# Kernel tuning notes

Hardware: AMD Instinct MI355X
Metric: run time of the kernel (lower is better)

## Reference

```python
import jax, jax.numpy as jnp
import numpy as np

VOCAB = 100000
EMBED = 300
HIDDEN = 300
BATCH = 32768
K_NEG = 10
N_CLASSES = 2
EPS = 1e-5
DENO_W = 1.0
CONO_W = 1.0


def setup_inputs() -> dict:
    key = jax.random.key(0)
    ks = jax.random.split(key, 12)
    init_range = 1.0 / EMBED
    return {
        "center_word_ids": jax.random.randint(ks[0], (BATCH,), 0, VOCAB),
        "context_word_ids": jax.random.randint(ks[1], (BATCH,), 0, VOCAB),
        "neg_context_ids": jax.random.randint(ks[2], (BATCH, K_NEG), 0, VOCAB),
        "party_label": jax.random.randint(ks[3], (BATCH,), 0, N_CLASSES),
        "center_emb": jax.random.uniform(ks[4], (VOCAB, EMBED), jnp.float32, -init_range, init_range),
        "context_emb": jax.random.normal(ks[5], (VOCAB, EMBED), jnp.float32) * 0.02,
        "W_enc": jax.random.normal(ks[6], (HIDDEN, EMBED), jnp.float32) * (1.0 / np.sqrt(EMBED)),
        "b_enc": jnp.zeros((HIDDEN,), jnp.float32),
        "W_dec": jax.random.normal(ks[7], (EMBED, HIDDEN), jnp.float32) * (1.0 / np.sqrt(HIDDEN)),
        "b_dec": jnp.zeros((EMBED,), jnp.float32),
        "W_cls": jax.random.normal(ks[8], (N_CLASSES, HIDDEN), jnp.float32) * (1.0 / np.sqrt(HIDDEN)),
        "b_cls": jnp.zeros((N_CLASSES,), jnp.float32),
    }


def reference(center_word_ids, context_word_ids, neg_context_ids, party_label,
              center_emb, context_emb, W_enc, b_enc, W_dec, b_dec, W_cls, b_cls):
    # encoder_forward (dropout p=0 -> identity)
    emb = center_emb[center_word_ids]                      # [B, E]
    enc = emb @ W_enc.T + b_enc                            # [B, H]
    # deno_forward: skip-gram negative sampling
    center_v = enc @ W_dec.T + b_dec                       # [B, E]
    ctx_v = context_emb[context_word_ids]                  # [B, E]
    pos_score = jnp.clip(jnp.sum(center_v * ctx_v, axis=1), -10.0, 10.0)
    pos = -jax.nn.log_sigmoid(pos_score)                   # [B]
    neg_v = context_emb[neg_context_ids]                   # [B, K, E]
    neg_score = jnp.clip(jnp.einsum('bke,be->bk', neg_v, center_v), -10.0, 10.0)
    neg = -jnp.sum(jax.nn.log_sigmoid(-neg_score), axis=1)  # [B]
    deno_loss = jnp.clip(jnp.mean(pos + neg), EPS, 10.0)
    # cono_forward + cross entropy
    logits = enc @ W_cls.T + b_cls                         # [B, C]
    logp = jax.nn.log_softmax(logits, axis=-1)
    nll = -jnp.take_along_axis(logp, party_label[:, None], axis=1)[:, 0]
    cono_loss = jnp.clip(jnp.mean(nll), EPS, 10.0)
    encoder_loss = jnp.clip(DENO_W * deno_loss + CONO_W * cono_loss, EPS, None)
    return jnp.stack([encoder_loss, deno_loss, cono_loss])
```

## Files before the change

### kernel.cpp

```cpp
#include <hip/hip_runtime.h>
#include <math.h>

#define VOCAB   100000
#define EMBED   300
#define HIDDEN  300
#define BATCH   32768
#define K_NEG   10
#define EPSV    1e-5f

#define KPAD      320
#define NPAD      384
#define CV_STRIDE 304
#define CTX8_STRIDE 304
#define WC2_STRIDE 304
#define FP8_SCALE 64.0f
#define FP8_DESCALE 0.015625f
#define NBUCKET 512

typedef __attribute__((ext_vector_type(8))) short  short8;
typedef __attribute__((ext_vector_type(4))) float  f32x4;
typedef __attribute__((ext_vector_type(2))) float  floatx2;

#if defined(__has_builtin)
#if __has_builtin(__builtin_amdgcn_cvt_pk_f32_fp8) && __has_builtin(__builtin_amdgcn_cvt_pk_fp8_f32)
#define HAVE_CVT_FP8 1
#endif
#endif

__device__ inline float b2f(unsigned short u) {
    union { unsigned int i; float f; } v; v.i = ((unsigned int)u) << 16; return v.f;
}
__device__ inline unsigned short f2b(float f) {
    union { float f; unsigned int i; } v; v.f = f;
    unsigned int r = v.i + 0x7FFFu + ((v.i >> 16) & 1u);
    return (unsigned short)(r >> 16);
}
__device__ inline void up2(unsigned int u, float& lo, float& hi) {
    union { unsigned int i; float f; } a, b;
    a.i = u << 16; b.i = u & 0xFFFF0000u;
    lo = a.f; hi = b.f;
}
__device__ inline float softplus_fast(float x) {
    const float t = __builtin_amdgcn_exp2f(fabsf(x) * -1.44269504f);
    const float l = __builtin_amdgcn_logf(1.f + t) * 0.69314718f;
    return fmaxf(x, 0.f) + l;
}

__device__ inline float fp8_to_f(unsigned int u8) {
    const unsigned s = (u8 >> 7) & 1, e = (u8 >> 3) & 15, m = u8 & 7;
    float v;
    if (e) { union { unsigned i; float f; } b; b.i = ((e + 120u) << 23) | (m << 20); v = b.f; }
    else v = (float)m * 0.001953125f;
    return s ? -v : v;
}
__device__ inline unsigned char f_to_fp8(float x) {
    union { float f; unsigned i; } b; b.f = x;
    const unsigned s = (b.i >> 31) << 7;
    const float a = fabsf(x);
    if (a >= 440.f) return (unsigned char)(s | 0x7E);
    if (a < 0.015625f) {
        int m = (int)rintf(a * 512.f);
        return (unsigned char)(m >= 8 ? (s | 0x08) : (s | (unsigned)m));
    }
    unsigned r = (b.i & 0x7FFFFFFFu) + 0x7FFFFu + ((b.i >> 20) & 1u);
    unsigned e8 = (r >> 23) - 120u;
    unsigned m8 = (r >> 20) & 7u;
    if (e8 > 15u) return (unsigned char)(s | 0x7E);
    return (unsigned char)(s | (e8 << 3) | m8);
}
__device__ inline unsigned enc4fp8(float a, float b, float c, float d) {
#ifdef HAVE_CVT_FP8
    int v = 0;
    v = __builtin_amdgcn_cvt_pk_fp8_f32(a, b, v, false);
    v = __builtin_amdgcn_cvt_pk_fp8_f32(c, d, v, true);
    return (unsigned)v;
#else
    return (unsigned)f_to_fp8(a) | ((unsigned)f_to_fp8(b) << 8) |
           ((unsigned)f_to_fp8(c) << 16) | ((unsigned)f_to_fp8(d) << 24);
#endif
}
__device__ inline void dec4fp8(unsigned u, float* f) {
#ifdef HAVE_CVT_FP8
    floatx2 lo = __builtin_amdgcn_cvt_pk_f32_fp8((int)u, false);
    floatx2 hi = __builtin_amdgcn_cvt_pk_f32_fp8((int)u, true);
    f[0] = lo[0]; f[1] = lo[1]; f[2] = hi[0]; f[3] = hi[1];
#else
    f[0] = fp8_to_f(u); f[1] = fp8_to_f(u >> 8);
    f[2] = fp8_to_f(u >> 16); f[3] = fp8_to_f(u >> 24);
#endif
}

__device__ inline void load_lds16(const void* g, void* l) {
    __builtin_amdgcn_global_load_lds(
        (const __attribute__((address_space(1))) unsigned int*)g,
        (__attribute__((address_space(3))) unsigned int*)l, 16, 0, 0);
}

__device__ inline float red64(float v) {
    #pragma unroll
    for (int m = 32; m; m >>= 1) v += __shfl_xor(v, m);
    return v;
}

#define CH1 (BATCH * 75)
#define CH2 (VOCAB * 75)
#define CHTOT (CH1 + CH2)
#define PREP_BLOCKS 2048

__global__ __launch_bounds__(256)
void prep_kernel(const float* __restrict__ cemb, const int* __restrict__ cids,
                 const float* __restrict__ xemb,
                 unsigned short* __restrict__ emb_b, unsigned char* __restrict__ ctx8)
{
    const unsigned GT = PREP_BLOCKS * 256;
    for (unsigned base = blockIdx.x * 256 + threadIdx.x; base < CHTOT; base += GT * 4) {
        float4 v[4];
        unsigned c[4];
        bool ok[4];
        #pragma unroll
        for (int u = 0; u < 4; ++u) {
            c[u] = base + u * GT;
            ok[u] = (c[u] < CHTOT);
            if (ok[u]) {
                unsigned cc = c[u];
                if (cc < CH1) {
                    const unsigned row = cc / 75, e = cc - row * 75;
                    v[u] = *(const float4*)(cemb + (size_t)cids[row] * 300 + e * 4);
                } else {
                    cc -= CH1;
                    const unsigned row = cc / 75, e = cc - row * 75;
                    v[u] = *(const float4*)(xemb + (size_t)row * 300 + e * 4);
                }
            }
        }
        #pragma unroll
        for (int u = 0; u < 4; ++u) {
            if (!ok[u]) continue;
            unsigned cc = c[u];
            if (cc < CH1) {
                const unsigned row = cc / 75, e = cc - row * 75;
                uint2 d;
                d.x = (unsigned)f2b(v[u].x) | ((unsigned)f2b(v[u].y) << 16);
                d.y = (unsigned)f2b(v[u].z) | ((unsigned)f2b(v[u].w) << 16);
                char* dst = (char*)emb_b + (size_t)row * (KPAD * 2) + e * 8;
                if (e < 74) {
                    *(uint2*)dst = d;
                } else {
                    *(uint4*)dst = make_uint4(d.x, d.y, 0u, 0u);
                    char* rb = (char*)emb_b + (size_t)row * (KPAD * 2);
                    *(uint4*)(rb + 608) = make_uint4(0u, 0u, 0u, 0u);
                    *(uint4*)(rb + 624) = make_uint4(0u, 0u, 0u, 0u);
                }
            } else {
                cc -= CH1;
                const unsigned row = cc / 75, e = cc - row * 75;
                const unsigned enc = enc4fp8(v[u].x * FP8_SCALE, v[u].y * FP8_SCALE,
                                             v[u].z * FP8_SCALE, v[u].w * FP8_SCALE);
                char* dst = (char*)ctx8 + (size_t)row * CTX8_STRIDE + e * 4;
                if (e < 74) {
                    *(unsigned*)dst = enc;
                } else {
                    *(uint2*)dst = make_uint2(enc, 0u);
                }
            }
        }
    }
}

__global__ __launch_bounds__(256)
void w2_kernel(const float* __restrict__ Wd, const float* __restrict__ We,
               unsigned short* __restrict__ w2p)
{
    __shared__ float ds[16][33];
    __shared__ float es[32][17];
    const int tid = threadIdx.x;
    const int tn = tid >> 4, tk = tid & 15;
    const int n = blockIdx.y * 16 + tn;
    const int k = blockIdx.x * 16 + tk;

    float acc = 0.f;
    for (int h0 = 0; h0 < 300; h0 += 32) {
        {
            const int i = tid * 2;
            const int a = i >> 5, h = i & 31;
            const int rr = blockIdx.y * 16 + a;
            #pragma unroll
            for (int j = 0; j < 2; ++j) {
                const int hh = h + j;
                ds[a][hh] = (rr < 300 && h0 + hh < 300) ? Wd[rr * 300 + h0 + hh] : 0.f;
            }
        }
        {
            const int i = tid * 2;
            const int h = i >> 4, c = i & 15;
            const int cc = blockIdx.x * 16 + c;
            #pragma unroll
            for (int j = 0; j < 2; ++j)
                es[h][c + j] = (h0 + h < 300 && cc + j < 300) ? We[(h0 + h) * 300 + cc + j] : 0.f;
        }
        __syncthreads();
        #pragma unroll
        for (int h = 0; h < 32; ++h)
            acc = fmaf(ds[tn][h], es[h][tk], acc);
        __syncthreads();
    }
    if (n < NPAD && k < KPAD)
        w2p[n * KPAD + k] = (n < 300 && k < 300) ? f2b(acc) : (unsigned short)0;
}

__global__ __launch_bounds__(256)
void wb_kernel(const float* __restrict__ Wd, const float* __restrict__ We,
               const float* __restrict__ Wc, const float* __restrict__ b_enc,
               const float* __restrict__ b_dec, const float* __restrict__ b_cls,
               float* __restrict__ wc2, float* __restrict__ bias2, float* __restrict__ bc2)
{
    const int unit = blockIdx.x * 4 + (threadIdx.x >> 6);
    const int lane = threadIdx.x & 63;
    if (unit >= 914) return;
    float s = 0.f;
    if (unit < 304) {
        const int c = unit;
        if (c < 300)
            for (int k = lane; k < 300; k += 64) s = fmaf(Wd[c * 300 + k], b_enc[k], s);
        s = red64(s);
        if (lane == 0) bias2[c] = (c < 300) ? s + b_dec[c] : 0.f;
    } else if (unit < 912) {
        const int u2 = unit - 304;
        const int j = u2 >= 304 ? 1 : 0;
        const int c = u2 - j * 304;
        if (c < 300)
            for (int h = lane; h < 300; h += 64) s = fmaf(Wc[j * 300 + h], We[h * 300 + c], s);
        s = red64(s);
        if (lane == 0) wc2[j * WC2_STRIDE + c] = s;
    } else {
        const int j = unit - 912;
        for (int h = lane; h < 300; h += 64) s = fmaf(Wc[j * 300 + h], b_enc[h], s);
        s = red64(s);
        if (lane == 0) bc2[j] = s + b_cls[j];
    }
}

__global__ __launch_bounds__(256)
void gemm_cv_kernel(const unsigned short* __restrict__ A,
                    const unsigned short* __restrict__ B,
                    const float* __restrict__ bias,
                    unsigned short* __restrict__ C)
{
    __shared__ unsigned short As[2][128 * 32];
    __shared__ unsigned short Bs[2][128 * 32];

    const int tid  = threadIdx.x;
    const int wave = tid >> 6;
    const int lane = tid & 63;
    const int m0 = blockIdx.y * 128;
    const int n0 = blockIdx.x * 128;

    const int wr = (wave & 1) * 64;
    const int wc = (wave >> 1) * 64;
    const int fr = lane & 15;
    const int fq = lane >> 4;

    const unsigned short* gA[2];
    const unsigned short* gB[2];
    int ldsOff[2];
    #pragma unroll
    for (int inst = 0; inst < 2; ++inst) {
        const int t = wave * 2 + inst;
        const int r = (t << 4) + (lane >> 2);
        const int c = ((lane & 3) - r - (r >> 2)) & 3;
        gA[inst] = A + (size_t)(m0 + r) * KPAD + c * 8;
        gB[inst] = B + (size_t)(n0 + r) * KPAD + c * 8;
        ldsOff[inst] = t << 9;
    }

    int aoff[4], boff[4];
    #pragma unroll
    for (int i = 0; i < 4; ++i) {
        const int ra = wr + i * 16 + fr;
        aoff[i] = (ra << 5) + (((fq + ra + (ra >> 2)) & 3) << 3);
        const int rb = wc + i * 16 + fr;
        boff[i] = (rb << 5) + (((fq + rb + (rb >> 2)) & 3) << 3);
    }

    f32x4 acc[4][4] = {};

    #pragma unroll
    for (int inst = 0; inst < 2; ++inst) {
        load_lds16(gA[inst], &As[0][ldsOff[inst]]);
        load_lds16(gB[inst], &Bs[0][ldsOff[inst]]);
    }

    int cur = 0;
    for (int ki = 0; ki < KPAD / 32; ++ki) {
        __syncthreads();
        if (ki + 1 < KPAD / 32) {
            const int k0 = (ki + 1) * 32;
            #pragma unroll
            for (int inst = 0; inst < 2; ++inst) {
                load_lds16(gA[inst] + k0, &As[cur ^ 1][ldsOff[inst]]);
                load_lds16(gB[inst] + k0, &Bs[cur ^ 1][ldsOff[inst]]);
            }
        }
        short8 af[4], bf[4];
        #pragma unroll
        for (int i = 0; i < 4; ++i) af[i] = *(const short8*)&As[cur][aoff[i]];
        #pragma unroll
        for (int j = 0; j < 4; ++j) bf[j] = *(const short8*)&Bs[cur][boff[j]];
        #pragma unroll
        for (int i = 0; i < 4; ++i)
            #pragma unroll
            for (int j = 0; j < 4; ++j)
                acc[i][j] = __builtin_amdgcn_mfma_f32_16x16x32_bf16(
                    af[i], bf[j], acc[i][j], 0, 0, 0);
        cur ^= 1;
    }

    #pragma unroll
    for (int i = 0; i < 4; ++i) {
        #pragma unroll
        for (int r = 0; r < 4; ++r) {
            const int m = m0 + wr + i * 16 + fq * 4 + r;
            unsigned short* crow = C + (size_t)m * CV_STRIDE;
            #pragma unroll
            for (int j = 0; j < 4; ++j) {
                const int n = n0 + wc + j * 16 + fr;
                if (n < 300) {
                    crow[n] = f2b(acc[i][j][r] + bias[n]);
                } else if (n < CV_STRIDE) {
                    crow[n] = 0;
                }
            }
        }
    }
}

__global__ __launch_bounds__(256)
void score_kernel(const unsigned short* __restrict__ cvb,
                  const unsigned char* __restrict__ ctx8,
                  const int* __restrict__ ctx_ids, const int* __restrict__ neg_ids,
                  float* __restrict__ db)
{
    const int wid  = threadIdx.x >> 6;
    const int lane = threadIdx.x & 63;
    const int fr = lane & 15;
    const int fq = lane >> 4;
    const int r0 = (blockIdx.x * 4 + wid) * 16;
    const int myrow = r0 + fr;

    union { uint4 u; short8 v; } z16; z16.u = make_uint4(0, 0, 0, 0);

    short8 af[10];
    const unsigned short* arow = cvb + (size_t)myrow * CV_STRIDE + fq * 8;
    #pragma unroll
    for (int kk = 0; kk < 10; ++kk) {
        if (kk < 9 || fq < 2) af[kk] = *(const short8*)(arow + kk * 32);
        else af[kk] = z16.v;
    }

    int ids[11];
    ids[0] = ctx_ids[myrow];
    #pragma unroll
    for (int j = 0; j < 10; ++j) ids[j + 1] = neg_ids[myrow * K_NEG + j];

    const bool dlane = (fr >> 2) == fq;
    const int  dreg  = fr & 3;
    float loss = 0.f;

    #pragma unroll
    for (int j = 0; j < 11; ++j) {
        const unsigned char* brow = ctx8 + (size_t)ids[j] * CTX8_STRIDE + fq * 8;
        f32x4 acc = {};
        #pragma unroll
        for (int kk = 0; kk < 10; ++kk) {
            uint2 u;
            if (kk < 9 || fq < 2) u = *(const uint2*)(brow + kk * 32);
            else u = make_uint2(0, 0);
            float f[8];
            dec4fp8(u.x, f); dec4fp8(u.y, f + 4);
            union { unsigned w[4]; short8 v; } bf;
            union { float ff; unsigned ii; } p0, p1, p2, p3, p4, p5, p6, p7;
            p0.ff = f[0]; p1.ff = f[1]; p2.ff = f[2]; p3.ff = f[3];
            p4.ff = f[4]; p5.ff = f[5]; p6.ff = f[6]; p7.ff = f[7];
            bf.w[0] = (p1.ii & 0xFFFF0000u) | (p0.ii >> 16);
            bf.w[1] = (p3.ii & 0xFFFF0000u) | (p2.ii >> 16);
            bf.w[2] = (p5.ii & 0xFFFF0000u) | (p4.ii >> 16);
            bf.w[3] = (p7.ii & 0xFFFF0000u) | (p6.ii >> 16);
            acc = __builtin_amdgcn_mfma_f32_16x16x32_bf16(af[kk], bf.v, acc, 0, 0, 0);
        }
        if (dlane) {
            float dv = (dreg & 2) ? ((dreg & 1) ? acc[3] : acc[2])
                                  : ((dreg & 1) ? acc[1] : acc[0]);
            float s = dv * FP8_DESCALE;
            s = fminf(10.f, fmaxf(-10.f, s));
            loss += softplus_fast(j == 0 ? -s : s);
        }
    }

    float v = red64(loss);
    if (lane == 0) atomicAdd(&db[blockIdx.x & (NBUCKET - 1)], v);
}

__global__ __launch_bounds__(256)
void ce_kernel(const unsigned short* __restrict__ embb,
               const int* __restrict__ labels,
               const float* __restrict__ wc2, const float* __restrict__ bc2,
               float* __restrict__ cb)
{
    const int wid  = threadIdx.x >> 6;
    const int lane = threadIdx.x & 63;
    const int l5   = lane & 31;
    const int row  = blockIdx.x * 8 + wid * 2 + (lane >> 5);
    const bool act = l5 < 19;

    const uint4 Z4 = make_uint4(0, 0, 0, 0);
    const char* evp = (const char*)(embb + (size_t)row * KPAD);
    uint4 e0 = act ? *(const uint4*)(evp + l5 * 32)      : Z4;
    uint4 e1 = act ? *(const uint4*)(evp + l5 * 32 + 16) : Z4;
    float ev[16];
    up2(e0.x, ev[0], ev[1]);  up2(e0.y, ev[2], ev[3]);
    up2(e0.z, ev[4], ev[5]);  up2(e0.w, ev[6], ev[7]);
    up2(e1.x, ev[8], ev[9]);  up2(e1.y, ev[10], ev[11]);
    up2(e1.z, ev[12], ev[13]);up2(e1.w, ev[14], ev[15]);

    float p0 = 0.f, p1 = 0.f;
    if (act) {
        const float* w0 = wc2 + l5 * 16;
        const float* w1 = wc2 + WC2_STRIDE + l5 * 16;
        #pragma unroll
        for (int q = 0; q < 4; ++q) {
            float4 a = *(const float4*)(w0 + q * 4);
            float4 c = *(const float4*)(w1 + q * 4);
            p0 = fmaf(ev[q*4], a.x, p0); p0 = fmaf(ev[q*4+1], a.y, p0);
            p0 = fmaf(ev[q*4+2], a.z, p0); p0 = fmaf(ev[q*4+3], a.w, p0);
            p1 = fmaf(ev[q*4], c.x, p1); p1 = fmaf(ev[q*4+1], c.y, p1);
            p1 = fmaf(ev[q*4+2], c.z, p1); p1 = fmaf(ev[q*4+3], c.w, p1);
        }
    }
    #pragma unroll
    for (int m = 16; m; m >>= 1) { p0 += __shfl_xor(p0, m); p1 += __shfl_xor(p1, m); }

    if (l5 == 0) {
        const float l0 = p0 + bc2[0];
        const float l1 = p1 + bc2[1];
        const float mx = fmaxf(l0, l1);
        const float lse = mx + logf(expf(l0 - mx) + expf(l1 - mx));
        const float nll = lse - (labels[row] ? l1 : l0);
        atomicAdd(&cb[blockIdx.x & (NBUCKET - 1)], nll);
    }
}

__device__ inline float wave_red64(float v) {
    #pragma unroll
    for (int o = 32; o; o >>= 1) v += __shfl_down(v, o);
    return v;
}
__global__ __launch_bounds__(256)
void finalize_kernel(const float* __restrict__ db, const float* __restrict__ cb,
                     float* __restrict__ out)
{
    const int t = threadIdx.x;
    float d = db[t] + db[t + 256];
    float c = cb[t] + cb[t + 256];
    d = wave_red64(d); c = wave_red64(c);
    __shared__ float sd[4], sc[4];
    if ((t & 63) == 0) { sd[t >> 6] = d; sc[t >> 6] = c; }
    __syncthreads();
    if (t == 0) {
        const float inv = 1.0f / (float)BATCH;
        float deno = (sd[0] + sd[1] + sd[2] + sd[3]) * inv;
        float cono = (sc[0] + sc[1] + sc[2] + sc[3]) * inv;
        deno = fminf(10.f, fmaxf(EPSV, deno));
        cono = fminf(10.f, fmaxf(EPSV, cono));
        out[0] = fmaxf(EPSV, deno + cono);
        out[1] = deno;
        out[2] = cono;
    }
}

extern "C" void kernel_launch(void* const* d_in, const int* in_sizes, int n_in,
                              void* d_out, int out_size, void* d_ws, size_t ws_size,
                              hipStream_t stream)
{
    const int*   cids  = (const int*)d_in[0];
    const int*   ctx   = (const int*)d_in[1];
    const int*   neg   = (const int*)d_in[2];
    const int*   lab   = (const int*)d_in[3];
    const float* cemb  = (const float*)d_in[4];
    const float* xemb  = (const float*)d_in[5];
    const float* W_enc = (const float*)d_in[6];
    const float* b_enc = (const float*)d_in[7];
    const float* W_dec = (const float*)d_in[8];
    const float* b_dec = (const float*)d_in[9];
    const float* W_cls = (const float*)d_in[10];
    const float* b_cls = (const float*)d_in[11];
    float* out = (float*)d_out;

    unsigned short* emb_b = (unsigned short*)d_ws;
    unsigned short* cv_b  = emb_b + (size_t)BATCH * KPAD;
    unsigned char*  ctx8  = (unsigned char*)(cv_b + (size_t)BATCH * CV_STRIDE);
    unsigned short* w2p   = (unsigned short*)(ctx8 + (size_t)VOCAB * CTX8_STRIDE);
    float* wc2   = (float*)(w2p + (size_t)NPAD * KPAD);
    float* bias2 = wc2 + 2 * WC2_STRIDE;
    float* bc2   = bias2 + WC2_STRIDE;
    float* db    = bc2 + 4;
    float* cb    = db + NBUCKET;

    hipMemsetAsync(db, 0, 2 * NBUCKET * sizeof(float), stream);

    prep_kernel<<<PREP_BLOCKS, 256, 0, stream>>>(cemb, cids, xemb, emb_b, ctx8);

    dim3 wgrid(KPAD / 16, NPAD / 16);
    w2_kernel<<<wgrid, 256, 0, stream>>>(W_dec, W_enc, w2p);
    wb_kernel<<<229, 256, 0, stream>>>(W_dec, W_enc, W_cls, b_enc, b_dec, b_cls,
                                       wc2, bias2, bc2);

    dim3 ggrid(3, BATCH / 128);
    gemm_cv_kernel<<<ggrid, 256, 0, stream>>>(emb_b, w2p, bias2, cv_b);

    score_kernel<<<BATCH / 64, 256, 0, stream>>>(cv_b, ctx8, ctx, neg, db);
    ce_kernel<<<BATCH / 8, 256, 0, stream>>>(emb_b, lab, wc2, bc2, cb);

    finalize_kernel<<<1, 256, 0, stream>>>(db, cb, out);
}
```

Before: 360.9 us.

## Gather fp32 context rows directly in score kernel, drop fp8 table conversion

The prep kernel no longer converts the whole 100000x300 context embedding table to fp8 on every call; it now only gathers and packs the center embeddings to bf16. The score kernel reads fp32 context rows straight from the input and truncates them to bf16 in registers before the MFMA, so the fp8 decode and the scale and descale steps go away. This removes a full read and write pass over the large table. In exchange, each gathered row is four times larger, which raises the score kernel's random-gather traffic and leans more on cache reuse of the 120 MB table.

```diff
diff --git a/kernel.cpp b/kernel.cpp
--- a/kernel.cpp
+++ b/kernel.cpp
@@ -11,25 +11,12 @@
 #define KPAD      320
 #define NPAD      384
 #define CV_STRIDE 304
-#define CTX8_STRIDE 304
 #define WC2_STRIDE 304
-#define FP8_SCALE 64.0f
-#define FP8_DESCALE 0.015625f
 #define NBUCKET 512
 
 typedef __attribute__((ext_vector_type(8))) short  short8;
 typedef __attribute__((ext_vector_type(4))) float  f32x4;
-typedef __attribute__((ext_vector_type(2))) float  floatx2;
-
-#if defined(__has_builtin)
-#if __has_builtin(__builtin_amdgcn_cvt_pk_f32_fp8) && __has_builtin(__builtin_amdgcn_cvt_pk_fp8_f32)
-#define HAVE_CVT_FP8 1
-#endif
-#endif
-
-__device__ inline float b2f(unsigned short u) {
-    union { unsigned int i; float f; } v; v.i = ((unsigned int)u) << 16; return v.f;
-}
+
 __device__ inline unsigned short f2b(float f) {
     union { float f; unsigned int i; } v; v.f = f;
     unsigned int r = v.i + 0x7FFFu + ((v.i >> 16) & 1u);
@@ -46,50 +33,6 @@
     return fmaxf(x, 0.f) + l;
 }
 
-__device__ inline float fp8_to_f(unsigned int u8) {
-    const unsigned s = (u8 >> 7) & 1, e = (u8 >> 3) & 15, m = u8 & 7;
-    float v;
-    if (e) { union { unsigned i; float f; } b; b.i = ((e + 120u) << 23) | (m << 20); v = b.f; }
-    else v = (float)m * 0.001953125f;
-    return s ? -v : v;
-}
-__device__ inline unsigned char f_to_fp8(float x) {
-    union { float f; unsigned i; } b; b.f = x;
-    const unsigned s = (b.i >> 31) << 7;
-    const float a = fabsf(x);
-    if (a >= 440.f) return (unsigned char)(s | 0x7E);
-    if (a < 0.015625f) {
-        int m = (int)rintf(a * 512.f);
-        return (unsigned char)(m >= 8 ? (s | 0x08) : (s | (unsigned)m));
-    }
-    unsigned r = (b.i & 0x7FFFFFFFu) + 0x7FFFFu + ((b.i >> 20) & 1u);
-    unsigned e8 = (r >> 23) - 120u;
-    unsigned m8 = (r >> 20) & 7u;
-    if (e8 > 15u) return (unsigned char)(s | 0x7E);
-    return (unsigned char)(s | (e8 << 3) | m8);
-}
-__device__ inline unsigned enc4fp8(float a, float b, float c, float d) {
-#ifdef HAVE_CVT_FP8
-    int v = 0;
-    v = __builtin_amdgcn_cvt_pk_fp8_f32(a, b, v, false);
-    v = __builtin_amdgcn_cvt_pk_fp8_f32(c, d, v, true);
-    return (unsigned)v;
-#else
-    return (unsigned)f_to_fp8(a) | ((unsigned)f_to_fp8(b) << 8) |
-           ((unsigned)f_to_fp8(c) << 16) | ((unsigned)f_to_fp8(d) << 24);
-#endif
-}
-__device__ inline void dec4fp8(unsigned u, float* f) {
-#ifdef HAVE_CVT_FP8
-    floatx2 lo = __builtin_amdgcn_cvt_pk_f32_fp8((int)u, false);
-    floatx2 hi = __builtin_amdgcn_cvt_pk_f32_fp8((int)u, true);
-    f[0] = lo[0]; f[1] = lo[1]; f[2] = hi[0]; f[3] = hi[1];
-#else
-    f[0] = fp8_to_f(u); f[1] = fp8_to_f(u >> 8);
-    f[2] = fp8_to_f(u >> 16); f[3] = fp8_to_f(u >> 24);
-#endif
-}
-
 __device__ inline void load_lds16(const void* g, void* l) {
     __builtin_amdgcn_global_load_lds(
         (const __attribute__((address_space(1))) unsigned int*)g,
@@ -102,66 +45,42 @@
     return v;
 }
 
-#define CH1 (BATCH * 75)
-#define CH2 (VOCAB * 75)
-#define CHTOT (CH1 + CH2)
+#define NCH (BATCH * 75)
 #define PREP_BLOCKS 2048
 
 __global__ __launch_bounds__(256)
 void prep_kernel(const float* __restrict__ cemb, const int* __restrict__ cids,
-                 const float* __restrict__ xemb,
-                 unsigned short* __restrict__ emb_b, unsigned char* __restrict__ ctx8)
+                 unsigned short* __restrict__ emb_b)
 {
     const unsigned GT = PREP_BLOCKS * 256;
-    for (unsigned base = blockIdx.x * 256 + threadIdx.x; base < CHTOT; base += GT * 4) {
+    for (unsigned base = blockIdx.x * 256 + threadIdx.x; base < NCH; base += GT * 4) {
         float4 v[4];
         unsigned c[4];
         bool ok[4];
         #pragma unroll
         for (int u = 0; u < 4; ++u) {
             c[u] = base + u * GT;
-            ok[u] = (c[u] < CHTOT);
+            ok[u] = (c[u] < NCH);
             if (ok[u]) {
-                unsigned cc = c[u];
-                if (cc < CH1) {
-                    const unsigned row = cc / 75, e = cc - row * 75;
-                    v[u] = *(const float4*)(cemb + (size_t)cids[row] * 300 + e * 4);
-                } else {
-                    cc -= CH1;
-                    const unsigned row = cc / 75, e = cc - row * 75;
-                    v[u] = *(const float4*)(xemb + (size_t)row * 300 + e * 4);
-                }
+                const unsigned row = c[u] / 75, e = c[u] - row * 75;
+                v[u] = *(const float4*)(cemb + (size_t)cids[row] * 300 + e * 4);
             }
         }
         #pragma unroll
         for (int u = 0; u < 4; ++u) {
             if (!ok[u]) continue;
-            unsigned cc = c[u];
-            if (cc < CH1) {
-                const unsigned row = cc / 75, e = cc - row * 75;
-                uint2 d;
-                d.x = (unsigned)f2b(v[u].x) | ((unsigned)f2b(v[u].y) << 16);
-                d.y = (unsigned)f2b(v[u].z) | ((unsigned)f2b(v[u].w) << 16);
-                char* dst = (char*)emb_b + (size_t)row * (KPAD * 2) + e * 8;
-                if (e < 74) {
-                    *(uint2*)dst = d;
-                } else {
-                    *(uint4*)dst = make_uint4(d.x, d.y, 0u, 0u);
-                    char* rb = (char*)emb_b + (size_t)row * (KPAD * 2);
-                    *(uint4*)(rb + 608) = make_uint4(0u, 0u, 0u, 0u);
-                    *(uint4*)(rb + 624) = make_uint4(0u, 0u, 0u, 0u);
-                }
+            const unsigned row = c[u] / 75, e = c[u] - row * 75;
+            uint2 d;
+            d.x = (unsigned)f2b(v[u].x) | ((unsigned)f2b(v[u].y) << 16);
+            d.y = (unsigned)f2b(v[u].z) | ((unsigned)f2b(v[u].w) << 16);
+            char* dst = (char*)emb_b + (size_t)row * (KPAD * 2) + e * 8;
+            if (e < 74) {
+                *(uint2*)dst = d;
             } else {
-                cc -= CH1;
-                const unsigned row = cc / 75, e = cc - row * 75;
-                const unsigned enc = enc4fp8(v[u].x * FP8_SCALE, v[u].y * FP8_SCALE,
-                                             v[u].z * FP8_SCALE, v[u].w * FP8_SCALE);
-                char* dst = (char*)ctx8 + (size_t)row * CTX8_STRIDE + e * 4;
-                if (e < 74) {
-                    *(unsigned*)dst = enc;
-                } else {
-                    *(uint2*)dst = make_uint2(enc, 0u);
-                }
+                *(uint4*)dst = make_uint4(d.x, d.y, 0u, 0u);
+                char* rb = (char*)emb_b + (size_t)row * (KPAD * 2);
+                *(uint4*)(rb + 608) = make_uint4(0u, 0u, 0u, 0u);
+                *(uint4*)(rb + 624) = make_uint4(0u, 0u, 0u, 0u);
             }
         }
     }
@@ -336,7 +255,7 @@
 
 __global__ __launch_bounds__(256)
 void score_kernel(const unsigned short* __restrict__ cvb,
-                  const unsigned char* __restrict__ ctx8,
+                  const float* __restrict__ xemb,
                   const int* __restrict__ ctx_ids, const int* __restrict__ neg_ids,
                   float* __restrict__ db)
 {
@@ -344,8 +263,7 @@
     const int lane = threadIdx.x & 63;
     const int fr = lane & 15;
     const int fq = lane >> 4;
-    const int r0 = (blockIdx.x * 4 + wid) * 16;
-    const int myrow = r0 + fr;
+    const int myrow = (blockIdx.x * 4 + wid) * 16 + fr;
 
     union { uint4 u; short8 v; } z16; z16.u = make_uint4(0, 0, 0, 0);
 
@@ -368,30 +286,33 @@
 
     #pragma unroll
     for (int j = 0; j < 11; ++j) {
-        const unsigned char* brow = ctx8 + (size_t)ids[j] * CTX8_STRIDE + fq * 8;
+        const float* brow = xemb + (size_t)ids[j] * 300;
         f32x4 acc = {};
         #pragma unroll
         for (int kk = 0; kk < 10; ++kk) {
-            uint2 u;
-            if (kk < 9 || fq < 2) u = *(const uint2*)(brow + kk * 32);
-            else u = make_uint2(0, 0);
-            float f[8];
-            dec4fp8(u.x, f); dec4fp8(u.y, f + 4);
+            const int kb = kk * 32 + fq * 8;
+            uint4 u0, u1;
+            if (kk < 9 || fq == 0) {
+                u0 = *(const uint4*)(brow + kb);
+                u1 = *(const uint4*)(brow + kb + 4);
+            } else if (fq == 1) {
+                u0 = *(const uint4*)(brow + 296);
+                u1 = make_uint4(0, 0, 0, 0);
+            } else {
+                u0 = make_uint4(0, 0, 0, 0);
+                u1 = make_uint4(0, 0, 0, 0);
+            }
             union { unsigned w[4]; short8 v; } bf;
-            union { float ff; unsigned ii; } p0, p1, p2, p3, p4, p5, p6, p7;
-            p0.ff = f[0]; p1.ff = f[1]; p2.ff = f[2]; p3.ff = f[3];
-            p4.ff = f[4]; p5.ff = f[5]; p6.ff = f[6]; p7.ff = f[7];
-            bf.w[0] = (p1.ii & 0xFFFF0000u) | (p0.ii >> 16);
-            bf.w[1] = (p3.ii & 0xFFFF0000u) | (p2.ii >> 16);
-            bf.w[2] = (p5.ii & 0xFFFF0000u) | (p4.ii >> 16);
-            bf.w[3] = (p7.ii & 0xFFFF0000u) | (p6.ii >> 16);
+            bf.w[0] = (u0.y & 0xFFFF0000u) | (u0.x >> 16);
+            bf.w[1] = (u0.w & 0xFFFF0000u) | (u0.z >> 16);
+            bf.w[2] = (u1.y & 0xFFFF0000u) | (u1.x >> 16);
+            bf.w[3] = (u1.w & 0xFFFF0000u) | (u1.z >> 16);
             acc = __builtin_amdgcn_mfma_f32_16x16x32_bf16(af[kk], bf.v, acc, 0, 0, 0);
         }
         if (dlane) {
             float dv = (dreg & 2) ? ((dreg & 1) ? acc[3] : acc[2])
                                   : ((dreg & 1) ? acc[1] : acc[0]);
-            float s = dv * FP8_DESCALE;
-            s = fminf(10.f, fmaxf(-10.f, s));
+            float s = fminf(10.f, fmaxf(-10.f, dv));
             loss += softplus_fast(j == 0 ? -s : s);
         }
     }
@@ -497,8 +418,7 @@
 
     unsigned short* emb_b = (unsigned short*)d_ws;
     unsigned short* cv_b  = emb_b + (size_t)BATCH * KPAD;
-    unsigned char*  ctx8  = (unsigned char*)(cv_b + (size_t)BATCH * CV_STRIDE);
-    unsigned short* w2p   = (unsigned short*)(ctx8 + (size_t)VOCAB * CTX8_STRIDE);
+    unsigned short* w2p   = cv_b + (size_t)BATCH * CV_STRIDE;
     float* wc2   = (float*)(w2p + (size_t)NPAD * KPAD);
     float* bias2 = wc2 + 2 * WC2_STRIDE;
     float* bc2   = bias2 + WC2_STRIDE;
@@ -507,7 +427,7 @@
 
     hipMemsetAsync(db, 0, 2 * NBUCKET * sizeof(float), stream);
 
-    prep_kernel<<<PREP_BLOCKS, 256, 0, stream>>>(cemb, cids, xemb, emb_b, ctx8);
+    prep_kernel<<<PREP_BLOCKS, 256, 0, stream>>>(cemb, cids, emb_b);
 
     dim3 wgrid(KPAD / 16, NPAD / 16);
     w2_kernel<<<wgrid, 256, 0, stream>>>(W_dec, W_enc, w2p);
@@ -517,7 +437,7 @@
     dim3 ggrid(3, BATCH / 128);
     gemm_cv_kernel<<<ggrid, 256, 0, stream>>>(emb_b, w2p, bias2, cv_b);
 
-    score_kernel<<<BATCH / 64, 256, 0, stream>>>(cv_b, ctx8, ctx, neg, db);
+    score_kernel<<<BATCH / 64, 256, 0, stream>>>(cv_b, xemb, ctx, neg, db);
     ce_kernel<<<BATCH / 8, 256, 0, stream>>>(emb_b, lab, wc2, bc2, cb);
 
     finalize_kernel<<<1, 256, 0, stream>>>(db, cb, out);
```

Measured after the change: 374.9 us. +3.9%, slower.
